# Performance work log

Hardware: AMD Instinct MI355X
Metric: run time of the kernel (lower is better)

Reference implementation:

```python
import jax, jax.numpy as jnp
import numpy as np

N_NODES = 100000
N_EDGES = 1600000
IN_CH = 128
HID = 128
N_REL = 8


def setup_inputs() -> dict:
    key = jax.random.key(0)
    k_x, k_src, k_dst, k_et, k_w, k_root, k_b = jax.random.split(key, 7)
    x = jax.random.normal(k_x, (N_NODES, IN_CH), dtype=jnp.float32)
    src = jax.random.randint(k_src, (N_EDGES,), 0, N_NODES)
    dst = jax.random.randint(k_dst, (N_EDGES,), 0, N_NODES)
    edge_index = jnp.stack([src, dst], axis=0)  # [2, E]
    edge_type = jax.random.randint(k_et, (N_EDGES,), 0, N_REL)
    # RGCNConv parameters: per-relation weight, root (self-loop) weight, bias
    scale = 1.0 / np.sqrt(IN_CH)
    W = jax.random.normal(k_w, (N_REL, IN_CH, HID), dtype=jnp.float32) * scale
    root = jax.random.normal(k_root, (IN_CH, HID), dtype=jnp.float32) * scale
    bias = jnp.zeros((HID,), dtype=jnp.float32)
    return {"x": x, "edge_index": edge_index, "edge_type": edge_type,
            "W": W, "root": root, "bias": bias}


def reference(x, edge_index, edge_type, W, root, bias):
    # RGCNConv (mean aggregation per relation) + ReLU. Dropout is identity (eval mode).
    # Aggregate-then-transform: mathematically identical to PyG's
    # transform-then-aggregate since the relation transform is linear,
    # but far cheaper (R matmuls over N nodes instead of E edges).
    N = x.shape[0]
    n_rel = W.shape[0]
    src, dst = edge_index[0], edge_index[1]
    x_src = x[src]  # [E, C] gathered neighbor features
    out = x @ root + bias  # root / self-loop term
    for r in range(n_rel):
        mask = (edge_type == r)
        xm = jnp.where(mask[:, None], x_src, 0.0)  # zero out other relations
        agg = jax.ops.segment_sum(xm, dst, num_segments=N)  # [N, C]
        cnt = jax.ops.segment_sum(mask.astype(x.dtype), dst, num_segments=N)
        mean_agg = agg / jnp.maximum(cnt, 1.0)[:, None]
        out = out + mean_agg @ W[r]
    return jax.nn.relu(out)
```

## Files before the change

kernel.cpp:

```cpp
#include <hip/hip_runtime.h>

#define NREL 8
#define CH   128
#define YW   1152
#define YWD  (YW / 2)
#define NCB2 18

#define SCAN_THREADS 256
#define NSC_ITEMS    4
#define NSC_CHUNK    1024
#define NSC_SHIFT    10

typedef short  short8v __attribute__((ext_vector_type(8)));
typedef float  f32x4   __attribute__((ext_vector_type(4)));

__device__ __forceinline__ unsigned short f2bf(float f) {
    union { float f; unsigned u; } v; v.f = f;
    return (unsigned short)((v.u + 0x7FFFu + ((v.u >> 16) & 1u)) >> 16);
}
__device__ __forceinline__ float lof(unsigned u) {
    union { unsigned u; float f; } v; v.u = u << 16; return v.f;
}
__device__ __forceinline__ float hif(unsigned u) {
    union { unsigned u; float f; } v; v.u = u & 0xFFFF0000u; return v.f;
}
__device__ __forceinline__ void gload_lds16(const void* g, void* l) {
    __builtin_amdgcn_global_load_lds(
        (const __attribute__((address_space(1))) unsigned int*)g,
        (__attribute__((address_space(3))) unsigned int*)l, 16, 0, 0);
}

__global__ __launch_bounds__(256) void bt2_kernel(
    const float* __restrict__ W, const float* __restrict__ root,
    unsigned short* __restrict__ Bt2)
{
    int idx = blockIdx.x * blockDim.x + threadIdx.x;
    if (idx >= YW * CH) return;
    int rc = idx >> 7, k = idx & 127;
    int r = rc >> 7, c = rc & 127;
    float v = (r < NREL) ? W[(size_t)(r * CH + k) * CH + c]
                         : root[(size_t)k * CH + c];
    Bt2[idx] = f2bf(v);
}

__global__ __launch_bounds__(256) void hist_kernel(
    const int* __restrict__ dst, const int* __restrict__ et,
    int* __restrict__ hist, int E)
{
    int e = blockIdx.x * blockDim.x + threadIdx.x;
    if (e < E) atomicAdd(&hist[dst[e] * NREL + et[e]], 1);
}

__global__ __launch_bounds__(SCAN_THREADS) void scan1_kernel(
    const int* __restrict__ hist, int* __restrict__ nofs,
    int* __restrict__ partials, int N)
{
    __shared__ int lds[SCAN_THREADS];
    int t = threadIdx.x;
    int base = blockIdx.x * NSC_CHUNK + t * NSC_ITEMS;
    int v[NSC_ITEMS];
    int s = 0;
#pragma unroll
    for (int j = 0; j < NSC_ITEMS; j++) {
        int n = base + j;
        int deg = 0;
        if (n < N) {
            int4 a = *(const int4*)(hist + (size_t)n * NREL);
            int4 b = *(const int4*)(hist + (size_t)n * NREL + 4);
            deg = a.x + a.y + a.z + a.w + b.x + b.y + b.z + b.w;
        }
        v[j] = s; s += deg;
    }
    int run = s;
    lds[t] = run; __syncthreads();
    for (int off = 1; off < SCAN_THREADS; off <<= 1) {
        int y = (t >= off) ? lds[t - off] : 0;
        __syncthreads();
        run += y; lds[t] = run; __syncthreads();
    }
    int tb = run - s;
    if (t == SCAN_THREADS - 1) partials[blockIdx.x] = run;
#pragma unroll
    for (int j = 0; j < NSC_ITEMS; j++) {
        int n = base + j;
        if (n < N) nofs[n] = tb + v[j];
    }
}

__global__ __launch_bounds__(SCAN_THREADS) void scan2_kernel(
    int* __restrict__ partials, int NB)
{
    __shared__ int lds[SCAN_THREADS];
    int t = threadIdx.x;
    int s = (t < NB) ? partials[t] : 0;
    int run = s;
    lds[t] = run; __syncthreads();
    for (int off = 1; off < SCAN_THREADS; off <<= 1) {
        int y = (t >= off) ? lds[t - off] : 0;
        __syncthreads();
        run += y; lds[t] = run; __syncthreads();
    }
    if (t < NB) partials[t] = run - s;
}

__global__ __launch_bounds__(256) void finalize_kernel(
    int* __restrict__ nofs, const int* __restrict__ partials,
    int* __restrict__ pad_noffs, int N)
{
    int i = blockIdx.x * blockDim.x + threadIdx.x;
    if (i < N) nofs[i] += partials[i >> NSC_SHIFT];
    if (i == 0) pad_noffs[0] = 0;
}

__global__ __launch_bounds__(512, 6) void ygemm_fill_kernel(
    const float* __restrict__ x,
    const unsigned short* __restrict__ Bt2,
    unsigned short* __restrict__ y,
    int N,
    const int* __restrict__ src, const int* __restrict__ dst,
    const int* __restrict__ et, int* __restrict__ nofs,
    int* __restrict__ perm, int E, int epb)
{
    __shared__ __align__(16) unsigned short As[128 * 128];
    __shared__ __align__(16) unsigned short Bs[64 * 128];

    int tid  = threadIdx.x;
    int lane = tid & 63;
    int wid  = tid >> 6;
    int wm   = wid >> 2;
    int wn   = wid & 3;
    int r15  = lane & 15;
    int kg   = lane >> 4;
    int n0   = blockIdx.x * 128;

    int eb   = blockIdx.x * epb;
    int elim = eb + epb; if (elim > E) elim = E;
    int p0 = -1, p1 = -1, p2 = -1, p3 = -1;
    int v0 = 0, v1 = 0, v2 = 0, v3 = 0;
    {
        int e0 = eb + tid;
        int e1 = e0 + 512, e2 = e1 + 512, e3 = e2 + 512;
        if (e0 < elim) { v0 = (src[e0] << 3) | et[e0]; p0 = atomicAdd(&nofs[dst[e0]], 1); }
        if (e1 < elim) { v1 = (src[e1] << 3) | et[e1]; p1 = atomicAdd(&nofs[dst[e1]], 1); }
        if (e2 < elim) { v2 = (src[e2] << 3) | et[e2]; p2 = atomicAdd(&nofs[dst[e2]], 1); }
        if (e3 < elim) { v3 = (src[e3] << 3) | et[e3]; p3 = atomicAdd(&nofs[dst[e3]], 1); }
    }

    {
        int row = tid >> 2;
        int kq  = tid & 3;
        int gn  = n0 + row; if (gn >= N) gn = N - 1;
        const float* xp = x + (size_t)gn * CH + kq * 32;
#pragma unroll
        for (int s8 = 0; s8 < 4; ++s8) {
            float4 f0 = *(const float4*)(xp + s8 * 8);
            float4 f1 = *(const float4*)(xp + s8 * 8 + 4);
            uint4 v;
            v.x = f2bf(f0.x) | ((unsigned)f2bf(f0.y) << 16);
            v.y = f2bf(f0.z) | ((unsigned)f2bf(f0.w) << 16);
            v.z = f2bf(f1.x) | ((unsigned)f2bf(f1.y) << 16);
            v.w = f2bf(f1.z) | ((unsigned)f2bf(f1.w) << 16);
            int slot = kq * 4 + s8;
            int phys = slot ^ (row & 15);
            *(uint4*)&As[row * 128 + phys * 8] = v;
        }
    }

    if (p0 >= 0) perm[p0] = v0;
    if (p1 >= 0) perm[p1] = v1;
    if (p2 >= 0) perm[p2] = v2;
    if (p3 >= 0) perm[p3] = v3;

    for (int cb = 0; cb < NCB2; ++cb) {
#pragma unroll
        for (int i = 0; i < 2; ++i) {
            int chunk = wid * 2 + i;
            int col   = chunk * 4 + (lane >> 4);
            int slot  = (lane & 15) ^ (col & 15);
            const char* srcp = (const char*)(Bt2 + (size_t)(cb * 64 + col) * CH + slot * 8);
            gload_lds16(srcp, &Bs[chunk * 512]);
        }
        __syncthreads();

        f32x4 acc[4];
#pragma unroll
        for (int i = 0; i < 4; i++) acc[i] = f32x4{0.f, 0.f, 0.f, 0.f};

#pragma unroll
        for (int ks = 0; ks < 4; ++ks) {
            short8v a[4], b;
#pragma unroll
            for (int mr = 0; mr < 4; ++mr) {
                int row  = wm * 64 + mr * 16 + r15;
                int phys = (ks * 4 + kg) ^ (row & 15);
                a[mr] = *(const short8v*)&As[row * 128 + phys * 8];
            }
            {
                int col  = wn * 16 + r15;
                int phys = (ks * 4 + kg) ^ (col & 15);
                b = *(const short8v*)&Bs[col * 128 + phys * 8];
            }
#pragma unroll
            for (int mr = 0; mr < 4; ++mr)
                acc[mr] = __builtin_amdgcn_mfma_f32_16x16x32_bf16(
                    a[mr], b, acc[mr], 0, 0, 0);
        }

#pragma unroll
        for (int mr = 0; mr < 4; ++mr) {
#pragma unroll
            for (int reg = 0; reg < 4; ++reg) {
                int gr = n0 + wm * 64 + mr * 16 + kg * 4 + reg;
                if (gr >= N) continue;
                int gc = cb * 64 + wn * 16 + r15;
                y[(size_t)gr * YW + gc] = f2bf(acc[mr][reg]);
            }
        }
        __syncthreads();
    }
}

__global__ __launch_bounds__(256) void gather_kernel(
    const unsigned short* __restrict__ y,
    const int* __restrict__ perm,
    const int* __restrict__ pad_noffs,
    const int* __restrict__ hist,
    const float* __restrict__ bias,
    float* __restrict__ out, int N)
{
    int wid  = threadIdx.x >> 6;
    int lane = threadIdx.x & 63;
    int n    = blockIdx.x * 4 + wid;
    if (n >= N) return;

    int beg = pad_noffs[n];
    int end = pad_noffs[n + 1];

    int4 h0 = *(const int4*)(hist + (size_t)n * NREL);
    int4 h1 = *(const int4*)(hist + (size_t)n * NREL + 4);
    float iw0 = 1.0f / (float)max(h0.x, 1);
    float iw1 = 1.0f / (float)max(h0.y, 1);
    float iw2 = 1.0f / (float)max(h0.z, 1);
    float iw3 = 1.0f / (float)max(h0.w, 1);
    float iw4 = 1.0f / (float)max(h1.x, 1);
    float iw5 = 1.0f / (float)max(h1.y, 1);
    float iw6 = 1.0f / (float)max(h1.z, 1);
    float iw7 = 1.0f / (float)max(h1.w, 1);

    const unsigned* y32 = (const unsigned*)y;
    float a0 = 0.f, a1 = 0.f;

    for (int blk = beg; blk < end; blk += 64) {
        int m = end - blk; if (m > 64) m = 64;
        int   rv = 0;
        float wv = 0.f;
        if (lane < m) {
            int pv  = perm[blk + lane];
            int rel = pv & 7;
            rv = pv + (pv >> 3);
            float wa = (rel & 1) ? iw1 : iw0;
            float wb = (rel & 1) ? iw3 : iw2;
            float wc = (rel & 1) ? iw5 : iw4;
            float wd = (rel & 1) ? iw7 : iw6;
            float we_ = (rel & 2) ? wb : wa;
            float wf  = (rel & 2) ? wd : wc;
            wv = (rel & 4) ? wf : we_;
        }

        int j = 0;
#define EDGE_LOAD(K) \
            int   p##K = __shfl(rv, j + K);                     \
            float w##K = __shfl(wv, j + K);                     \
            unsigned u##K = y32[(size_t)p##K * 64 + lane];
#define EDGE_ACC(K) \
            a0 += w##K * lof(u##K); a1 += w##K * hif(u##K);

        for (; j + 16 <= m; j += 16) {
            EDGE_LOAD(0) EDGE_LOAD(1) EDGE_LOAD(2)  EDGE_LOAD(3)
            EDGE_LOAD(4) EDGE_LOAD(5) EDGE_LOAD(6)  EDGE_LOAD(7)
            EDGE_LOAD(8) EDGE_LOAD(9) EDGE_LOAD(10) EDGE_LOAD(11)
            EDGE_LOAD(12) EDGE_LOAD(13) EDGE_LOAD(14) EDGE_LOAD(15)
            EDGE_ACC(0)  EDGE_ACC(1)  EDGE_ACC(2)  EDGE_ACC(3)
            EDGE_ACC(4)  EDGE_ACC(5)  EDGE_ACC(6)  EDGE_ACC(7)
            EDGE_ACC(8)  EDGE_ACC(9)  EDGE_ACC(10) EDGE_ACC(11)
            EDGE_ACC(12) EDGE_ACC(13) EDGE_ACC(14) EDGE_ACC(15)
        }
        if (j + 8 <= m) {
            EDGE_LOAD(0) EDGE_LOAD(1) EDGE_LOAD(2) EDGE_LOAD(3)
            EDGE_LOAD(4) EDGE_LOAD(5) EDGE_LOAD(6) EDGE_LOAD(7)
            EDGE_ACC(0) EDGE_ACC(1) EDGE_ACC(2) EDGE_ACC(3)
            EDGE_ACC(4) EDGE_ACC(5) EDGE_ACC(6) EDGE_ACC(7)
            j += 8;
        }
        if (j + 4 <= m) {
            EDGE_LOAD(0) EDGE_LOAD(1) EDGE_LOAD(2) EDGE_LOAD(3)
            EDGE_ACC(0) EDGE_ACC(1) EDGE_ACC(2) EDGE_ACC(3)
            j += 4;
        }
        for (; j < m; ++j) {
            EDGE_LOAD(0)
            EDGE_ACC(0)
        }
#undef EDGE_LOAD
#undef EDGE_ACC
    }

    unsigned ur = y32[(size_t)n * YWD + (NREL * CH / 2) + lane];
    float o0 = a0 + lof(ur) + bias[lane * 2];
    float o1 = a1 + hif(ur) + bias[lane * 2 + 1];
    float2 ov;
    ov.x = fmaxf(o0, 0.f);
    ov.y = fmaxf(o1, 0.f);
    *(float2*)(out + (size_t)n * CH + lane * 2) = ov;
}

extern "C" void kernel_launch(void* const* d_in, const int* in_sizes, int n_in,
                              void* d_out, int out_size, void* d_ws, size_t ws_size,
                              hipStream_t stream)
{
    const float* x    = (const float*)d_in[0];
    const int*   ei   = (const int*)d_in[1];
    const int*   et   = (const int*)d_in[2];
    const float* W    = (const float*)d_in[3];
    const float* root = (const float*)d_in[4];
    const float* bias = (const float*)d_in[5];
    float*       out  = (float*)d_out;

    int N = in_sizes[0] / CH;
    int E = in_sizes[2];
    const int* src = ei;
    const int* dst = ei + E;

    int S   = N * NREL;
    int NBn = (N + NSC_CHUNK - 1) / NSC_CHUNK;

    unsigned short* y   = (unsigned short*)d_ws;
    unsigned short* Bt2 = y + (size_t)N * YW;
    int* hist      = (int*)(Bt2 + (size_t)YW * CH);
    int* pad_noffs = hist + S;
    int* partials  = pad_noffs + N + 1;
    int* perm      = partials + 256;
    int* nofs      = pad_noffs + 1;

    hipMemsetAsync(hist, 0, (size_t)S * sizeof(int), stream);

    int egrid = (E + 255) / 256;
    int G     = (N + 127) / 128;
    int epb   = ((E + G - 1) / G + 2047) & ~2047;

    bt2_kernel<<<(YW * CH + 255) / 256, 256, 0, stream>>>(W, root, Bt2);
    hist_kernel<<<egrid, 256, 0, stream>>>(dst, et, hist, E);
    scan1_kernel<<<NBn, SCAN_THREADS, 0, stream>>>(hist, nofs, partials, N);
    scan2_kernel<<<1, SCAN_THREADS, 0, stream>>>(partials, NBn);
    finalize_kernel<<<(N + 255) / 256, 256, 0, stream>>>(nofs, partials, pad_noffs, N);
    ygemm_fill_kernel<<<G, 512, 0, stream>>>(x, Bt2, y, N,
                                             src, dst, et, nofs, perm, E, epb);
    gather_kernel<<<(N + 3) / 4, 256, 0, stream>>>(y, perm, pad_noffs, hist, bias, out, N);
}
```

Baseline: 313.3 us.

## Compute edge ranks in histogram pass and scan per (node, relation) offsets

The histogram kernel now keeps the atomicAdd return value as each edge's rank within its (dst, relation) bucket. The scan runs over all N*8 bucket counts instead of per-node degrees. The fill step inside the GEMM kernel can then place edges with a plain load and add instead of a second round of atomics on per-node counters, and it produces an order sorted by relation within each node. Perm stores are also spread across the first few GEMM column-block iterations to overlap them with the matrix work. In exchange there is an extra rank array of E ints to write and read, and the scan is eight times larger.

```diff
diff --git a/kernel.cpp b/kernel.cpp
--- a/kernel.cpp
+++ b/kernel.cpp
@@ -6,10 +6,10 @@
 #define YWD  (YW / 2)
 #define NCB2 18
 
+#define SCAN_ITEMS   16
 #define SCAN_THREADS 256
-#define NSC_ITEMS    4
-#define NSC_CHUNK    1024
-#define NSC_SHIFT    10
+#define SCAN_CHUNK   (SCAN_ITEMS * SCAN_THREADS)
+#define SCAN_SHIFT   12
 
 typedef short  short8v __attribute__((ext_vector_type(8)));
 typedef float  f32x4   __attribute__((ext_vector_type(4)));
@@ -43,33 +43,28 @@
     Bt2[idx] = f2bf(v);
 }
 
-__global__ __launch_bounds__(256) void hist_kernel(
+__global__ __launch_bounds__(256) void hist_rank_kernel(
     const int* __restrict__ dst, const int* __restrict__ et,
-    int* __restrict__ hist, int E)
+    int* __restrict__ hist, int* __restrict__ rank, int E)
 {
     int e = blockIdx.x * blockDim.x + threadIdx.x;
-    if (e < E) atomicAdd(&hist[dst[e] * NREL + et[e]], 1);
+    if (e < E) rank[e] = atomicAdd(&hist[dst[e] * NREL + et[e]], 1);
 }
 
 __global__ __launch_bounds__(SCAN_THREADS) void scan1_kernel(
-    const int* __restrict__ hist, int* __restrict__ nofs,
-    int* __restrict__ partials, int N)
+    const int* __restrict__ hist, int* __restrict__ pad_offs,
+    int* __restrict__ partials, int S)
 {
     __shared__ int lds[SCAN_THREADS];
     int t = threadIdx.x;
-    int base = blockIdx.x * NSC_CHUNK + t * NSC_ITEMS;
-    int v[NSC_ITEMS];
+    int base = blockIdx.x * SCAN_CHUNK + t * SCAN_ITEMS;
+    int v[SCAN_ITEMS];
     int s = 0;
 #pragma unroll
-    for (int j = 0; j < NSC_ITEMS; j++) {
-        int n = base + j;
-        int deg = 0;
-        if (n < N) {
-            int4 a = *(const int4*)(hist + (size_t)n * NREL);
-            int4 b = *(const int4*)(hist + (size_t)n * NREL + 4);
-            deg = a.x + a.y + a.z + a.w + b.x + b.y + b.z + b.w;
-        }
-        v[j] = s; s += deg;
+    for (int j = 0; j < SCAN_ITEMS; j++) {
+        int idx = base + j;
+        int h = (idx < S) ? hist[idx] : 0;
+        v[j] = s; s += h;
     }
     int run = s;
     lds[t] = run; __syncthreads();
@@ -81,9 +76,9 @@
     int tb = run - s;
     if (t == SCAN_THREADS - 1) partials[blockIdx.x] = run;
 #pragma unroll
-    for (int j = 0; j < NSC_ITEMS; j++) {
-        int n = base + j;
-        if (n < N) nofs[n] = tb + v[j];
+    for (int j = 0; j < SCAN_ITEMS; j++) {
+        int idx = base + j;
+        if (idx < S) pad_offs[idx] = tb + v[j];
     }
 }
 
@@ -104,12 +99,11 @@
 }
 
 __global__ __launch_bounds__(256) void finalize_kernel(
-    int* __restrict__ nofs, const int* __restrict__ partials,
-    int* __restrict__ pad_noffs, int N)
+    int* __restrict__ pad_offs, const int* __restrict__ partials, int S, int E)
 {
     int i = blockIdx.x * blockDim.x + threadIdx.x;
-    if (i < N) nofs[i] += partials[i >> NSC_SHIFT];
-    if (i == 0) pad_noffs[0] = 0;
+    if (i < S)       pad_offs[i] += partials[i >> SCAN_SHIFT];
+    else if (i == S) pad_offs[i] = E;
 }
 
 __global__ __launch_bounds__(512, 6) void ygemm_fill_kernel(
@@ -118,7 +112,8 @@
     unsigned short* __restrict__ y,
     int N,
     const int* __restrict__ src, const int* __restrict__ dst,
-    const int* __restrict__ et, int* __restrict__ nofs,
+    const int* __restrict__ et, const int* __restrict__ rank,
+    const int* __restrict__ pad_offs,
     int* __restrict__ perm, int E, int epb)
 {
     __shared__ __align__(16) unsigned short As[128 * 128];
@@ -140,10 +135,14 @@
     {
         int e0 = eb + tid;
         int e1 = e0 + 512, e2 = e1 + 512, e3 = e2 + 512;
-        if (e0 < elim) { v0 = (src[e0] << 3) | et[e0]; p0 = atomicAdd(&nofs[dst[e0]], 1); }
-        if (e1 < elim) { v1 = (src[e1] << 3) | et[e1]; p1 = atomicAdd(&nofs[dst[e1]], 1); }
-        if (e2 < elim) { v2 = (src[e2] << 3) | et[e2]; p2 = atomicAdd(&nofs[dst[e2]], 1); }
-        if (e3 < elim) { v3 = (src[e3] << 3) | et[e3]; p3 = atomicAdd(&nofs[dst[e3]], 1); }
+        if (e0 < elim) { int t0 = et[e0]; v0 = (src[e0] << 3) | t0;
+                         p0 = pad_offs[dst[e0] * NREL + t0] + rank[e0]; }
+        if (e1 < elim) { int t1 = et[e1]; v1 = (src[e1] << 3) | t1;
+                         p1 = pad_offs[dst[e1] * NREL + t1] + rank[e1]; }
+        if (e2 < elim) { int t2 = et[e2]; v2 = (src[e2] << 3) | t2;
+                         p2 = pad_offs[dst[e2] * NREL + t2] + rank[e2]; }
+        if (e3 < elim) { int t3 = et[e3]; v3 = (src[e3] << 3) | t3;
+                         p3 = pad_offs[dst[e3] * NREL + t3] + rank[e3]; }
     }
 
     {
@@ -166,11 +165,6 @@
         }
     }
 
-    if (p0 >= 0) perm[p0] = v0;
-    if (p1 >= 0) perm[p1] = v1;
-    if (p2 >= 0) perm[p2] = v2;
-    if (p3 >= 0) perm[p3] = v3;
-
     for (int cb = 0; cb < NCB2; ++cb) {
 #pragma unroll
         for (int i = 0; i < 2; ++i) {
@@ -181,6 +175,11 @@
             gload_lds16(srcp, &Bs[chunk * 512]);
         }
         __syncthreads();
+
+        if      (cb == 1) { if (p0 >= 0) perm[p0] = v0; }
+        else if (cb == 2) { if (p1 >= 0) perm[p1] = v1; }
+        else if (cb == 3) { if (p2 >= 0) perm[p2] = v2; }
+        else if (cb == 4) { if (p3 >= 0) perm[p3] = v3; }
 
         f32x4 acc[4];
 #pragma unroll
@@ -223,7 +222,7 @@
 __global__ __launch_bounds__(256) void gather_kernel(
     const unsigned short* __restrict__ y,
     const int* __restrict__ perm,
-    const int* __restrict__ pad_noffs,
+    const int* __restrict__ pad_offs,
     const int* __restrict__ hist,
     const float* __restrict__ bias,
     float* __restrict__ out, int N)
@@ -233,8 +232,8 @@
     int n    = blockIdx.x * 4 + wid;
     if (n >= N) return;
 
-    int beg = pad_noffs[n];
-    int end = pad_noffs[n + 1];
+    int beg = pad_offs[n * NREL];
+    int end = pad_offs[n * NREL + NREL];
 
     int4 h0 = *(const int4*)(hist + (size_t)n * NREL);
     int4 h1 = *(const int4*)(hist + (size_t)n * NREL + 4);
@@ -331,16 +330,16 @@
     const int* src = ei;
     const int* dst = ei + E;
 
-    int S   = N * NREL;
-    int NBn = (N + NSC_CHUNK - 1) / NSC_CHUNK;
+    int S  = N * NREL;
+    int NB = (S + SCAN_CHUNK - 1) / SCAN_CHUNK;
 
     unsigned short* y   = (unsigned short*)d_ws;
     unsigned short* Bt2 = y + (size_t)N * YW;
-    int* hist      = (int*)(Bt2 + (size_t)YW * CH);
-    int* pad_noffs = hist + S;
-    int* partials  = pad_noffs + N + 1;
-    int* perm      = partials + 256;
-    int* nofs      = pad_noffs + 1;
+    int* hist     = (int*)(Bt2 + (size_t)YW * CH);
+    int* pad_offs = hist + S;
+    int* partials = pad_offs + S + 1;
+    int* perm     = partials + 256;
+    int* rank     = perm + E;
 
     hipMemsetAsync(hist, 0, (size_t)S * sizeof(int), stream);
 
@@ -349,11 +348,12 @@
     int epb   = ((E + G - 1) / G + 2047) & ~2047;
 
     bt2_kernel<<<(YW * CH + 255) / 256, 256, 0, stream>>>(W, root, Bt2);
-    hist_kernel<<<egrid, 256, 0, stream>>>(dst, et, hist, E);
-    scan1_kernel<<<NBn, SCAN_THREADS, 0, stream>>>(hist, nofs, partials, N);
-    scan2_kernel<<<1, SCAN_THREADS, 0, stream>>>(partials, NBn);
-    finalize_kernel<<<(N + 255) / 256, 256, 0, stream>>>(nofs, partials, pad_noffs, N);
+    hist_rank_kernel<<<egrid, 256, 0, stream>>>(dst, et, hist, rank, E);
+    scan1_kernel<<<NB, SCAN_THREADS, 0, stream>>>(hist, pad_offs, partials, S);
+    scan2_kernel<<<1, SCAN_THREADS, 0, stream>>>(partials, NB);
+    finalize_kernel<<<(S + 256) / 256, 256, 0, stream>>>(pad_offs, partials, S, E);
     ygemm_fill_kernel<<<G, 512, 0, stream>>>(x, Bt2, y, N,
-                                             src, dst, et, nofs, perm, E, epb);
-    gather_kernel<<<(N + 3) / 4, 256, 0, stream>>>(y, perm, pad_noffs, hist, bias, out, N);
-}
+                                             src, dst, et, rank, pad_offs,
+                                             perm, E, epb);
+    gather_kernel<<<(N + 3) / 4, 256, 0, stream>>>(y, perm, pad_offs, hist, bias, out, N);
+}
```

Result: faster. 282.5 us (median of 2 runs) (-9.8%).
